# Kernel tuning notes

Measured on AMD Instinct MI355X. Metric: run time of the kernel, lower is better.

Reference implementation:

```python
import jax, jax.numpy as jnp
import numpy as np
from jax import lax

# Rotation permutations for a flattened 3x3 kernel (row-major, new_flat[t] = orig_flat[perm[t]]),
# transcribed literally from _rotate_kernel for n = angle//45 in {0,1,2,3}.
PERMS = np.array([
    [0, 1, 2, 3, 4, 5, 6, 7, 8],  # 0 deg (identity)
    [3, 0, 1, 6, 4, 2, 7, 8, 5],  # 45 deg: outer ring shifted one step
    [6, 3, 0, 7, 4, 1, 8, 5, 2],  # 90 deg clockwise
    [7, 6, 3, 8, 4, 0, 5, 2, 1],  # 135 deg
], dtype=np.int32)


def setup_inputs() -> dict:
    key = jax.random.key(0)
    k1, k2, k3 = jax.random.split(key, 3)
    B, Cin, Cout, H, W = 16, 64, 64, 128, 128
    x = jax.random.normal(k1, (B, Cin, H, W), dtype=jnp.float32)
    weight = jax.random.normal(k2, (Cout, Cin, 3, 3), dtype=jnp.float32)
    bias = jax.random.normal(k3, (Cout, 1, 1), dtype=jnp.float32)
    return {"x": x, "weight": weight, "bias": bias}


def reference(x, weight, bias):
    # x: [B, Cin, H, W]; weight: [Cout, Cin, 3, 3]; bias: [Cout, 1, 1]
    B, Cin, H, W = x.shape
    Cout = weight.shape[0]
    n_ang = PERMS.shape[0]

    # Build the 4 rotated kernel variants in one gather.
    wflat = weight.reshape(Cout, Cin, 9)
    # [Cout, Cin, n_ang, 9] -> [n_ang, Cout, Cin, 3, 3] -> merge angle into output channels
    wrot = wflat[:, :, jnp.asarray(PERMS)].transpose(2, 0, 1, 3).reshape(n_ang * Cout, Cin, 3, 3)

    # ZeroPad2d(stride=1) then valid 3x3 conv -> same spatial size.
    xp = jnp.pad(x, ((0, 0), (0, 0), (1, 1), (1, 1)))
    y = lax.conv_general_dilated(
        xp, wrot, window_strides=(1, 1), padding="VALID",
        dimension_numbers=("NCHW", "OIHW", "NCHW"))  # [B, n_ang*Cout, H, W]

    y = y.reshape(B, n_ang, Cout, H, W).transpose(1, 0, 2, 3, 4)  # [n_ang, B, Cout, H, W]
    return y + bias  # bias (Cout,1,1) broadcasts over trailing dims
```

## Files before the change

kernel.cpp:

```cpp
#include <hip/hip_runtime.h>


#define CIN 64
#define COUT 64
#define HH 128
#define WW 128
#define NB 16
#define HW (HH*WW)

typedef short bf16x8 __attribute__((ext_vector_type(8)));
typedef float f32x16 __attribute__((ext_vector_type(16)));
#define AS1 __attribute__((address_space(1)))
#define AS3 __attribute__((address_space(3)))

__device__ __constant__ unsigned DOFF_d[4][9] = {
  {0,16,32,8576,8592,8608,17152,17168,17184},
  {16,32,8608,0,8592,17184,8576,17152,17168},
  {32,8608,17184,16,8592,17168,0,8576,17152},
  {8608,17184,17168,32,8592,17152,16,0,8576},
};

static __device__ __forceinline__ unsigned short f2bf(float f) {
  unsigned u = __builtin_bit_cast(unsigned, f);
  return (unsigned short)((u + 0x7FFFu + ((u >> 16) & 1u)) >> 16);
}
static __device__ __forceinline__ unsigned pk2(float lo, float hi) {
  return (unsigned)f2bf(lo) | ((unsigned)f2bf(hi) << 16);
}

__global__ void build_A_kernel(const float* __restrict__ wgt,
                               const float* __restrict__ bias,
                               unsigned short* __restrict__ A) {
  const int e = blockIdx.x * 256 + threadIdx.x;
  const int j = e & 7;
  const int cm = (e >> 3) & 63;
  const int half = (e >> 9) & 1;
  const int kc = e >> 10;
  if (kc < 36) {
    const int s = kc >> 2, q = kc & 3;
    const int ci = q * 16 + half * 8 + j;
    A[e] = f2bf(wgt[(cm * CIN + ci) * 9 + s]);
  } else if (kc == 36) {
    A[e] = (half == 0 && j == 0) ? f2bf(bias[cm]) : (unsigned short)0;
  }
}

static __device__ __forceinline__ void lgkm_barrier() {
  asm volatile("s_waitcnt lgkmcnt(0)" ::: "memory");
  __builtin_amdgcn_s_barrier();
}

#define XS_SLOT 1072
#define XS_ROW  8576
#define XS_OFF  75776
#define LDS_BYTES (XS_OFF + 10 * XS_ROW)

__global__ __launch_bounds__(1024, 4) void aconv_v12_kernel(
    const float* __restrict__ x,
    const unsigned short* __restrict__ Ag,
    float* __restrict__ out)
{
  __shared__ __align__(16) unsigned char lds[LDS_BYTES];

  const int tid = threadIdx.x;
  const int lane = tid & 63;
  const int wid = tid >> 6;
  const int a   = wid >> 2;
  const int row = wid & 3;
  const int half = lane >> 5;
  const int ln = lane & 31;

  const int b   = blockIdx.x >> 4;
  const int rem = blockIdx.x & 15;
  const int hbase = rem * 8;

  const unsigned char* Agb = (const unsigned char*)Ag;
  AS3 unsigned char* ldsa = (AS3 unsigned char*)lds;

  unsigned doff[9];
  #pragma unroll
  for (int s = 0; s < 9; ++s) doff[s] = DOFF_d[a][s];

  #pragma unroll
  for (int j = 0; j < 5; ++j) {
    const int i = wid + j * 16;
    if (i < 74)
      __builtin_amdgcn_global_load_lds(
          (const AS1 unsigned*)(Agb + i * 1024 + lane * 16),
          (AS3 unsigned*)(ldsa + i * 1024), 16, 0, 0);
  }

  auto stage = [&](int w0) {
    #pragma unroll
    for (int i = 0; i < 6; ++i) {
      const int g = tid + i * 1024;
      if (g < 5280) {
        const int r    = g / 528;
        const int rest = g - r * 528;
        const int slot = rest / 66;
        const int wI   = rest - slot * 66;
        const int gh = hbase - 1 + r;
        const int gw = w0 - 1 + wI;
        const bool inb = ((unsigned)gh < HH) && ((unsigned)gw < WW);
        const float* xp = x + (size_t)(b * CIN + slot * 8) * HW + (size_t)gh * WW + gw;
        float v[8];
        #pragma unroll
        for (int q = 0; q < 8; ++q) v[q] = inb ? xp[(size_t)q * HW] : 0.f;
        uint4 u;
        u.x = pk2(v[0], v[1]); u.y = pk2(v[2], v[3]);
        u.z = pk2(v[4], v[5]); u.w = pk2(v[6], v[7]);
        *(uint4*)(lds + XS_OFF + r * XS_ROW + slot * XS_SLOT + wI * 16) = u;
      }
    }
  };

  const unsigned char* Asb = lds + (unsigned)(half * 1024 + ln * 16);
  const unsigned char* Bsb = lds + XS_OFF + (unsigned)(half * XS_SLOT + ln * 16);

  bf16x8 ob = (bf16x8)(short)0;
  if (half == 0) ob[0] = (short)0x3F80;

  auto tile = [&](int it, int w0) {
    const unsigned rowbyte = (unsigned)((it * 4 + row) * XS_ROW);

    f32x16 acc[2][2];
    #pragma unroll
    for (int mf = 0; mf < 2; ++mf)
      #pragma unroll
      for (int nf = 0; nf < 2; ++nf) acc[mf][nf] = (f32x16)(0.f);

    #pragma unroll
    for (int s = 0; s < 9; ++s) {
      const unsigned bjs = doff[s] + rowbyte;
      #pragma unroll
      for (int q = 0; q < 4; ++q) {
        const bf16x8 af0 = *(const bf16x8*)(Asb + (s * 4 + q) * 2048);
        const bf16x8 af1 = *(const bf16x8*)(Asb + (s * 4 + q) * 2048 + 512);
        const unsigned bb = bjs + (unsigned)(q * 2 * XS_SLOT);
        const bf16x8 bf0 = *(const bf16x8*)(Bsb + bb);
        const bf16x8 bf1 = *(const bf16x8*)(Bsb + bb + 512);
        acc[0][0] = __builtin_amdgcn_mfma_f32_32x32x16_bf16(af0, bf0, acc[0][0], 0, 0, 0);
        acc[0][1] = __builtin_amdgcn_mfma_f32_32x32x16_bf16(af0, bf1, acc[0][1], 0, 0, 0);
        acc[1][0] = __builtin_amdgcn_mfma_f32_32x32x16_bf16(af1, bf0, acc[1][0], 0, 0, 0);
        acc[1][1] = __builtin_amdgcn_mfma_f32_32x32x16_bf16(af1, bf1, acc[1][1], 0, 0, 0);
      }
    }
    {
      const bf16x8 af0 = *(const bf16x8*)(Asb + 36 * 2048);
      const bf16x8 af1 = *(const bf16x8*)(Asb + 36 * 2048 + 512);
      acc[0][0] = __builtin_amdgcn_mfma_f32_32x32x16_bf16(af0, ob, acc[0][0], 0, 0, 0);
      acc[0][1] = __builtin_amdgcn_mfma_f32_32x32x16_bf16(af0, ob, acc[0][1], 0, 0, 0);
      acc[1][0] = __builtin_amdgcn_mfma_f32_32x32x16_bf16(af1, ob, acc[1][0], 0, 0, 0);
      acc[1][1] = __builtin_amdgcn_mfma_f32_32x32x16_bf16(af1, ob, acc[1][1], 0, 0, 0);
    }

    const int hout = hbase + it * 4 + row;
    #pragma unroll
    for (int mf = 0; mf < 2; ++mf)
      #pragma unroll
      for (int nf = 0; nf < 2; ++nf) {
        const f32x16 v = acc[mf][nf];
        float* op = out + (((size_t)(a * NB + b) * COUT + mf * 32 + 4 * half) * HH
                           + hout) * WW + w0 + nf * 32 + ln;
        #pragma unroll
        for (int g = 0; g < 16; ++g)
          __builtin_nontemporal_store(v[g], op + (size_t)((g & 3) + 8 * (g >> 2)) * HW);
      }
  };

  stage(0);
  __syncthreads();

  tile(0, 0);
  tile(1, 0);

  lgkm_barrier();
  stage(64);
  lgkm_barrier();

  tile(0, 64);
  tile(1, 64);
}

extern "C" void kernel_launch(void* const* d_in, const int* in_sizes, int n_in,
                              void* d_out, int out_size, void* d_ws, size_t ws_size,
                              hipStream_t stream) {
  const float* x    = (const float*)d_in[0];
  const float* wgt  = (const float*)d_in[1];
  const float* bias = (const float*)d_in[2];
  float* out = (float*)d_out;
  unsigned short* A = (unsigned short*)d_ws;

  build_A_kernel<<<148, 256, 0, stream>>>(wgt, bias, A);
  aconv_v12_kernel<<<256, 1024, 0, stream>>>(x, A, out);
}
```

Measured before the change: 107.4 us.

## Stage full-width rows in a rolling 4-row LDS ring with register prefetch

```diff
diff --git a/kernel.cpp b/kernel.cpp
--- a/kernel.cpp
+++ b/kernel.cpp
@@ -13,11 +13,11 @@
 #define AS1 __attribute__((address_space(1)))
 #define AS3 __attribute__((address_space(3)))
 
-__device__ __constant__ unsigned DOFF_d[4][9] = {
-  {0,16,32,8576,8592,8608,17152,17168,17184},
-  {16,32,8608,0,8592,17184,8576,17152,17168},
-  {32,8608,17184,16,8592,17168,0,8576,17152},
-  {8608,17184,17168,32,8592,17152,16,0,8576},
+__device__ __constant__ unsigned APERM_d[4][9] = {
+  {0,8192,16384,24576,32768,40960,49152,57344,65536},
+  {24576,0,8192,49152,32768,16384,57344,65536,40960},
+  {49152,24576,0,57344,32768,8192,65536,40960,16384},
+  {57344,49152,24576,65536,32768,0,40960,16384,8192},
 };
 
 static __device__ __forceinline__ unsigned short f2bf(float f) {
@@ -45,17 +45,12 @@
   }
 }
 
-static __device__ __forceinline__ void lgkm_barrier() {
-  asm volatile("s_waitcnt lgkmcnt(0)" ::: "memory");
-  __builtin_amdgcn_s_barrier();
-}
-
-#define XS_SLOT 1072
-#define XS_ROW  8576
+#define XS_SLOT 2080
+#define XS_ROW  16640
 #define XS_OFF  75776
-#define LDS_BYTES (XS_OFF + 10 * XS_ROW)
-
-__global__ __launch_bounds__(1024, 4) void aconv_v12_kernel(
+#define LDS_BYTES (XS_OFF + 4 * XS_ROW)
+
+__global__ __launch_bounds__(1024, 4) void aconv_v13_kernel(
     const float* __restrict__ x,
     const unsigned short* __restrict__ Ag,
     float* __restrict__ out)
@@ -65,8 +60,9 @@
   const int tid = threadIdx.x;
   const int lane = tid & 63;
   const int wid = tid >> 6;
-  const int a   = wid >> 2;
-  const int row = wid & 3;
+  const int a   = __builtin_amdgcn_readfirstlane(wid >> 2);
+  const int row = __builtin_amdgcn_readfirstlane((wid >> 1) & 1);
+  const int wh  = __builtin_amdgcn_readfirstlane(wid & 1);
   const int half = lane >> 5;
   const int ln = lane & 31;
 
@@ -76,10 +72,7 @@
 
   const unsigned char* Agb = (const unsigned char*)Ag;
   AS3 unsigned char* ldsa = (AS3 unsigned char*)lds;
-
-  unsigned doff[9];
-  #pragma unroll
-  for (int s = 0; s < 9; ++s) doff[s] = DOFF_d[a][s];
+  const uint4 z4 = {0u, 0u, 0u, 0u};
 
   #pragma unroll
   for (int j = 0; j < 5; ++j) {
@@ -89,39 +82,54 @@
           (const AS1 unsigned*)(Agb + i * 1024 + lane * 16),
           (AS3 unsigned*)(ldsa + i * 1024), 16, 0, 0);
   }
-
-  auto stage = [&](int w0) {
-    #pragma unroll
-    for (int i = 0; i < 6; ++i) {
-      const int g = tid + i * 1024;
-      if (g < 5280) {
-        const int r    = g / 528;
-        const int rest = g - r * 528;
-        const int slot = rest / 66;
-        const int wI   = rest - slot * 66;
-        const int gh = hbase - 1 + r;
-        const int gw = w0 - 1 + wI;
-        const bool inb = ((unsigned)gh < HH) && ((unsigned)gw < WW);
-        const float* xp = x + (size_t)(b * CIN + slot * 8) * HW + (size_t)gh * WW + gw;
-        float v[8];
-        #pragma unroll
-        for (int q = 0; q < 8; ++q) v[q] = inb ? xp[(size_t)q * HW] : 0.f;
-        uint4 u;
-        u.x = pk2(v[0], v[1]); u.y = pk2(v[2], v[3]);
-        u.z = pk2(v[4], v[5]); u.w = pk2(v[6], v[7]);
-        *(uint4*)(lds + XS_OFF + r * XS_ROW + slot * XS_SLOT + wI * 16) = u;
-      }
-    }
-  };
+  if (tid < 64) {
+    const int rs = tid >> 4, cs = (tid >> 1) & 7, side = tid & 1;
+    *(uint4*)(lds + XS_OFF + rs * XS_ROW + cs * XS_SLOT + side * 129 * 16) = z4;
+  }
+
+  const int sslot = (tid >> 7) & 7;
+  const int swc   = tid & 127;
+  const float* sxb = x + (size_t)(b * CIN + sslot * 8) * HW + swc;
+  const unsigned sdstb = (unsigned)(XS_OFF + sslot * XS_SLOT + (1 + swc) * 16);
+
+  #pragma unroll
+  for (int i = 0; i < 4; ++i) {
+    const int gh = hbase - 1 + i;
+    const bool inb = (unsigned)gh < HH;
+    const float* xp = sxb + (size_t)gh * WW;
+    float v[8];
+    #pragma unroll
+    for (int q = 0; q < 8; ++q) v[q] = inb ? xp[(size_t)q * HW] : 0.f;
+    uint4 u;
+    u.x = pk2(v[0], v[1]); u.y = pk2(v[2], v[3]);
+    u.z = pk2(v[4], v[5]); u.w = pk2(v[6], v[7]);
+    *(uint4*)(lds + sdstb + i * XS_ROW) = u;
+  }
+  __syncthreads();
+
+  float gv[2][8];
+  #pragma unroll
+  for (int i = 0; i < 2; ++i) {
+    const int gh = hbase + 3 + i;
+    const bool inb = (unsigned)gh < HH;
+    const float* xp = sxb + (size_t)gh * WW;
+    #pragma unroll
+    for (int q = 0; q < 8; ++q) gv[i][q] = inb ? xp[(size_t)q * HW] : 0.f;
+  }
 
   const unsigned char* Asb = lds + (unsigned)(half * 1024 + ln * 16);
-  const unsigned char* Bsb = lds + XS_OFF + (unsigned)(half * XS_SLOT + ln * 16);
+  const unsigned char* Bsb = lds + XS_OFF + (unsigned)(half * XS_SLOT + (wh * 64 + ln) * 16);
 
   bf16x8 ob = (bf16x8)(short)0;
   if (half == 0) ob[0] = (short)0x3F80;
 
-  auto tile = [&](int it, int w0) {
-    const unsigned rowbyte = (unsigned)((it * 4 + row) * XS_ROW);
+  #pragma unroll 1
+  for (int it = 0; it < 4; ++it) {
+    const int rowbase = it * 2 + row;
+    unsigned ro[3];
+    #pragma unroll
+    for (int dh = 0; dh < 3; ++dh)
+      ro[dh] = (unsigned)(((rowbase + dh) & 3) * XS_ROW);
 
     f32x16 acc[2][2];
     #pragma unroll
@@ -130,13 +138,30 @@
       for (int nf = 0; nf < 2; ++nf) acc[mf][nf] = (f32x16)(0.f);
 
     #pragma unroll
-    for (int s = 0; s < 9; ++s) {
-      const unsigned bjs = doff[s] + rowbyte;
+    for (int t = 0; t < 9; ++t) {
+      if (t == 6) {
+        asm volatile("s_waitcnt lgkmcnt(0)" ::: "memory");
+        __builtin_amdgcn_s_barrier();
+        if (it < 3) {
+          #pragma unroll
+          for (int i = 0; i < 2; ++i) {
+            const int gh = hbase + it * 2 + 3 + i;
+            uint4 u = z4;
+            if (gh < HH) {
+              u.x = pk2(gv[i][0], gv[i][1]); u.y = pk2(gv[i][2], gv[i][3]);
+              u.z = pk2(gv[i][4], gv[i][5]); u.w = pk2(gv[i][6], gv[i][7]);
+            }
+            *(uint4*)(lds + sdstb + (unsigned)(((it * 2 + i) & 3) * XS_ROW)) = u;
+          }
+        }
+      }
+      const unsigned aoff = APERM_d[a][t];
+      const unsigned bbt = ro[t / 3] + (unsigned)((t % 3) * 16);
       #pragma unroll
       for (int q = 0; q < 4; ++q) {
-        const bf16x8 af0 = *(const bf16x8*)(Asb + (s * 4 + q) * 2048);
-        const bf16x8 af1 = *(const bf16x8*)(Asb + (s * 4 + q) * 2048 + 512);
-        const unsigned bb = bjs + (unsigned)(q * 2 * XS_SLOT);
+        const bf16x8 af0 = *(const bf16x8*)(Asb + aoff + q * 2048);
+        const bf16x8 af1 = *(const bf16x8*)(Asb + aoff + q * 2048 + 512);
+        const unsigned bb = bbt + (unsigned)(q * 2 * XS_SLOT);
         const bf16x8 bf0 = *(const bf16x8*)(Bsb + bb);
         const bf16x8 bf1 = *(const bf16x8*)(Bsb + bb + 512);
         acc[0][0] = __builtin_amdgcn_mfma_f32_32x32x16_bf16(af0, bf0, acc[0][0], 0, 0, 0);
@@ -154,32 +179,33 @@
       acc[1][1] = __builtin_amdgcn_mfma_f32_32x32x16_bf16(af1, ob, acc[1][1], 0, 0, 0);
     }
 
-    const int hout = hbase + it * 4 + row;
+    if (it < 2) {
+      #pragma unroll
+      for (int i = 0; i < 2; ++i) {
+        const int gh = hbase + it * 2 + 5 + i;
+        const bool inb = (unsigned)gh < HH;
+        const float* xp = sxb + (size_t)gh * WW;
+        #pragma unroll
+        for (int q = 0; q < 8; ++q) gv[i][q] = inb ? xp[(size_t)q * HW] : 0.f;
+      }
+    }
+
+    const int hout = hbase + it * 2 + row;
     #pragma unroll
     for (int mf = 0; mf < 2; ++mf)
       #pragma unroll
       for (int nf = 0; nf < 2; ++nf) {
         const f32x16 v = acc[mf][nf];
         float* op = out + (((size_t)(a * NB + b) * COUT + mf * 32 + 4 * half) * HH
-                           + hout) * WW + w0 + nf * 32 + ln;
+                           + hout) * WW + wh * 64 + nf * 32 + ln;
         #pragma unroll
         for (int g = 0; g < 16; ++g)
           __builtin_nontemporal_store(v[g], op + (size_t)((g & 3) + 8 * (g >> 2)) * HW);
       }
-  };
-
-  stage(0);
-  __syncthreads();
-
-  tile(0, 0);
-  tile(1, 0);
-
-  lgkm_barrier();
-  stage(64);
-  lgkm_barrier();
-
-  tile(0, 64);
-  tile(1, 64);
+
+    asm volatile("s_waitcnt lgkmcnt(0)" ::: "memory");
+    __builtin_amdgcn_s_barrier();
+  }
 }
 
 extern "C" void kernel_launch(void* const* d_in, const int* in_sizes, int n_in,
@@ -192,5 +218,5 @@
   unsigned short* A = (unsigned short*)d_ws;
 
   build_A_kernel<<<148, 256, 0, stream>>>(wgt, bias, A);
-  aconv_v12_kernel<<<256, 1024, 0, stream>>>(x, A, out);
-}
+  aconv_v13_kernel<<<256, 1024, 0, stream>>>(x, A, out);
+}
```

Result: no change. 107.7 us (+0.2%).
